# Optimization experiments

Measured on AMD Instinct MI355X. Metric: run time of the kernel, lower is better.

Reference implementation:

```python
import jax, jax.numpy as jnp
import numpy as np

T, B, D, H = 1024, 512, 128, 256


def setup_inputs() -> dict:
    key = jax.random.key(0)
    k0, k1, k2, k3, k4, k5 = jax.random.split(key, 6)
    data = jax.random.normal(k0, (T, B, D), dtype=jnp.float32)
    # ragged lengths in [1, T]; masked recurrence == packed-sequence semantics
    lengths = jax.random.randint(k1, (B,), 1, T + 1, dtype=jnp.int32)
    s_ih = 1.0 / np.sqrt(D)
    s_hh = 1.0 / np.sqrt(H)
    ih_w = jax.random.uniform(k2, (H, D), minval=-s_ih, maxval=s_ih, dtype=jnp.float32)
    ih_b = jax.random.uniform(k3, (H,), minval=-s_ih, maxval=s_ih, dtype=jnp.float32)
    hh_w = jax.random.uniform(k4, (2 * H, H), minval=-s_hh, maxval=s_hh, dtype=jnp.float32)
    hh_b = jax.random.uniform(k5, (2 * H,), minval=-s_hh, maxval=s_hh, dtype=jnp.float32)
    return {"data": data, "ih_w": ih_w, "ih_b": ih_b, "hh_w": hh_w, "hh_b": hh_b, "lengths": lengths}


def reference(data, ih_w, ih_b, hh_w, hh_b, lengths):
    # data: [T, B, D]; masked update replicates packed-sequence 'first size rows' semantics
    Tn, Bn, _ = data.shape
    Hn = ih_w.shape[0]

    def step(hidden, inp):
        x_t, t = inp
        hid = hidden @ hh_w.T + hh_b                    # [B, 2H]
        alpha, h = jnp.split(hid, 2, axis=1)
        alpha = jax.nn.sigmoid(alpha)
        h = (jnp.exp2(alpha * h) - 1.0) / alpha + alpha  # soft-exp gate
        new_hidden = jnp.tanh(x_t @ ih_w.T + ih_b + h)   # [B, H]
        valid = (t < lengths)[:, None]
        return jnp.where(valid, new_hidden, hidden), None

    h0 = jnp.zeros((Bn, Hn), dtype=data.dtype)
    hidden, _ = jax.lax.scan(step, h0, (data, jnp.arange(Tn)))
    return hidden[None]  # [1, B, H], matching hidden.unsqueeze(0)
```

## Files before the change

### kernel.cpp

```cpp
#include <hip/hip_runtime.h>


#define BB 512
#define DD 128
#define HH 256

typedef __attribute__((ext_vector_type(8))) short bf16x8;
typedef __attribute__((ext_vector_type(4))) float f32x4;

static __device__ __forceinline__ short f2bf(float f) {
    unsigned u = __float_as_uint(f);
    u += 0x7FFFu + ((u >> 16) & 1u);
    return (short)(u >> 16);
}
static __device__ __forceinline__ bf16x8 pack8(const float4 a, const float4 b) {
    bf16x8 v;
    v[0] = f2bf(a.x); v[1] = f2bf(a.y); v[2] = f2bf(a.z); v[3] = f2bf(a.w);
    v[4] = f2bf(b.x); v[5] = f2bf(b.y); v[6] = f2bf(b.z); v[7] = f2bf(b.w);
    return v;
}

__global__ __launch_bounds__(1024, 4)
void rnn_fused(const float* __restrict__ data, const float* __restrict__ ih_w,
               const float* __restrict__ ih_b, const float* __restrict__ hh_w,
               const float* __restrict__ hh_b, const int* __restrict__ lengths,
               float* __restrict__ out)
{
    const int g    = blockIdx.x;
    const int tid  = threadIdx.x;
    const int w    = tid >> 6;
    const int lane = tid & 63;
    const int col  = lane & 15;
    const int quad = lane >> 4;

    __shared__ short hbuf[2][32][4][8];
    __shared__ short dbuf[2][2][DD];

    bf16x8 whh[2][8];
    #pragma unroll
    for (int s = 0; s < 2; ++s) {
        const int wrow = s*HH + 16*w + col;
        const float* src = hh_w + wrow * HH;
        #pragma unroll
        for (int i = 0; i < 8; ++i) {
            const float4 a = *(const float4*)(src + i*32 + quad*8);
            const float4 b = *(const float4*)(src + i*32 + quad*8 + 4);
            whh[s][i] = pack8(a, b);
        }
    }
    bf16x8 wih[4];
    {
        const int wrow = 16*w + col;
        const float* src = ih_w + wrow * DD;
        #pragma unroll
        for (int i = 0; i < 4; ++i) {
            const float4 a = *(const float4*)(src + i*32 + quad*8);
            const float4 b = *(const float4*)(src + i*32 + quad*8 + 4);
            wih[i] = pack8(a, b);
        }
    }

    const float bA = hh_b[      16*w + col];
    const float bH = hh_b[HH  + 16*w + col];
    const float bX = ih_b[      16*w + col];

    const int L0 = lengths[2*g];
    const int L1 = lengths[2*g + 1];
    const int Lmax = (L0 > L1) ? L0 : L1;

    const bool smine = (quad == 0);
    const int  se    = (w << 4) | col;

    for (int idx = tid; idx < 32*4*8; idx += 1024)
        ((short*)hbuf[0])[idx] = 0;
    if (smine)
        ((short*)dbuf[0])[se] = f2bf(data[(size_t)(2*g) * DD + se]);
    float vstage = 0.f;
    if (smine && 1 < Lmax)
        vstage = data[((size_t)1 * BB + 2*g) * DD + se];
    __syncthreads();

    float  nh[2] = {0.f, 0.f};
    bf16x8 frag[4] = {};

    const bool acth = (col < 4);
    const bool actd = (col < 2);

    for (int t = 0; t < Lmax; ++t) {
        const int p = t & 1;

        if (smine && t + 1 < Lmax)
            ((short*)dbuf[1 - p])[se] = f2bf(vstage);
        float vnew = 0.f;
        if (smine && t + 2 < Lmax)
            vnew = data[((size_t)(t+2) * BB + 2*g) * DD + se];

        f32x4 racc[2] = {{0.f,0.f,0.f,0.f},{0.f,0.f,0.f,0.f}};
        #pragma unroll
        for (int half = 0; half < 2; ++half) {
            if (acth) {
                #pragma unroll
                for (int i = 0; i < 4; ++i)
                    frag[i] = *(const bf16x8*)
                        &hbuf[p][(half*4 + i)*4 + quad][col][0];
            }
            #pragma unroll
            for (int i = 0; i < 4; ++i)
                #pragma unroll
                for (int s = 0; s < 2; ++s)
                    racc[s] = __builtin_amdgcn_mfma_f32_16x16x32_bf16(
                        frag[i], whh[s][half*4 + i], racc[s], 0, 0, 0);
        }

        if (actd) {
            #pragma unroll
            for (int i = 0; i < 4; ++i)
                frag[i] = *(const bf16x8*)&dbuf[p][col][i*32 + quad*8];
        }
        f32x4 xacc = {0.f, 0.f, 0.f, 0.f};
        #pragma unroll
        for (int i = 0; i < 4; ++i)
            xacc = __builtin_amdgcn_mfma_f32_16x16x32_bf16(
                frag[i], wih[i], xacc, 0, 0, 0);

        float vres[2];
        #pragma unroll
        for (int r = 0; r < 2; ++r) {
            const float a   = racc[0][r] + racc[0][2 + r] + bA;
            const float hv  = racc[1][r] + racc[1][2 + r] + bH;
            const float e   = __builtin_amdgcn_exp2f(a * -1.4426950408889634f);
            const float inv = 1.0f + e;
            const float al  = __builtin_amdgcn_rcpf(inv);
            const float xs  = xacc[r] + bX;
            const float c1  = al + xs - inv;
            const float pp  = __builtin_amdgcn_exp2f(al * hv);
            const float u   = __builtin_fmaf(pp, inv, c1);
            const float t2  = __builtin_amdgcn_exp2f(u * 2.8853900817779268f);
            const float th  = 1.0f - 2.0f * __builtin_amdgcn_rcpf(1.0f + t2);
            const int   Lr  = r ? L1 : L0;
            vres[r] = (t < Lr) ? th : nh[r];
            nh[r]   = vres[r];
        }

        unsigned pkhi, pklo;
        asm("v_cvt_pk_bf16_f32 %0, %1, %2"
            : "=v"(pkhi) : "v"(vres[0]), "v"(vres[1]));
        const float b0 = __uint_as_float(pkhi << 16);
        const float b1 = __uint_as_float(pkhi & 0xFFFF0000u);
        asm("v_cvt_pk_bf16_f32 %0, %1, %2"
            : "=v"(pklo) : "v"(vres[0] - b0), "v"(vres[1] - b1));
        if (quad == 0) {
            const int c = 16*w + col;
            short* hb = &hbuf[1 - p][c >> 3][0][c & 7];
            hb[0]  = (short)(pkhi & 0xFFFFu);
            hb[8]  = (short)(pkhi >> 16);
            hb[16] = (short)(pklo & 0xFFFFu);
            hb[24] = (short)(pklo >> 16);
        }

        vstage = vnew;
        __syncthreads();
    }

    if (quad == 0) {
        #pragma unroll
        for (int r = 0; r < 2; ++r)
            out[(size_t)(2*g + r) * HH + 16*w + col] = nh[r];
    }
}

extern "C" void kernel_launch(void* const* d_in, const int* in_sizes, int n_in,
                              void* d_out, int out_size, void* d_ws, size_t ws_size,
                              hipStream_t stream) {
    const float* data    = (const float*)d_in[0];
    const float* ih_w    = (const float*)d_in[1];
    const float* ih_b    = (const float*)d_in[2];
    const float* hh_w    = (const float*)d_in[3];
    const float* hh_b    = (const float*)d_in[4];
    const int*   lengths = (const int*)d_in[5];
    float* out = (float*)d_out;

    (void)in_sizes; (void)n_in; (void)out_size; (void)d_ws; (void)ws_size;

    rnn_fused<<<dim3(BB / 2), dim3(1024), 0, stream>>>(
        data, ih_w, ih_b, hh_w, hh_b, lengths, out);
}
```

Before: 1.341 ms.

## Split per-row gate math across quads via swizzle, add MFMA priority and lighter barrier

The element-wise activation chain, which ran serially for two batch rows in quad 0 of each wave, is now split so quads 0 and 1 each handle one row. A ds_swizzle moves the second row's accumulator values across lanes, which halves the transcendental latency on the recurrent critical path. MFMA sections are wrapped in s_setprio, and __syncthreads is replaced by an explicit lgkmcnt wait plus s_barrier to cut barrier overhead. The cost is extra swizzle instructions, and the hand-written barrier relies on correct waitcnt semantics.

```diff
diff --git a/kernel.cpp b/kernel.cpp
--- a/kernel.cpp
+++ b/kernel.cpp
@@ -18,6 +18,10 @@
     v[0] = f2bf(a.x); v[1] = f2bf(a.y); v[2] = f2bf(a.z); v[3] = f2bf(a.w);
     v[4] = f2bf(b.x); v[5] = f2bf(b.y); v[6] = f2bf(b.z); v[7] = f2bf(b.w);
     return v;
+}
+static __device__ __forceinline__ float swz16(float x) {
+    return __uint_as_float((unsigned)__builtin_amdgcn_ds_swizzle(
+        (int)__float_as_uint(x), 0x401F));
 }
 
 __global__ __launch_bounds__(1024, 4)
@@ -80,11 +84,13 @@
         vstage = data[((size_t)1 * BB + 2*g) * DD + se];
     __syncthreads();
 
-    float  nh[2] = {0.f, 0.f};
+    float  nhv = 0.f;
     bf16x8 frag[4] = {};
 
     const bool acth = (col < 4);
     const bool actd = (col < 2);
+    const int  rq   = quad & 1;
+    const int  Lr   = rq ? L1 : L0;
 
     for (int t = 0; t < Lmax; ++t) {
         const int p = t & 1;
@@ -96,6 +102,7 @@
             vnew = data[((size_t)(t+2) * BB + 2*g) * DD + se];
 
         f32x4 racc[2] = {{0.f,0.f,0.f,0.f},{0.f,0.f,0.f,0.f}};
+        __builtin_amdgcn_s_setprio(1);
         #pragma unroll
         for (int half = 0; half < 2; ++half) {
             if (acth) {
@@ -122,51 +129,49 @@
         for (int i = 0; i < 4; ++i)
             xacc = __builtin_amdgcn_mfma_f32_16x16x32_bf16(
                 frag[i], wih[i], xacc, 0, 0, 0);
+        __builtin_amdgcn_s_setprio(0);
 
-        float vres[2];
-        #pragma unroll
-        for (int r = 0; r < 2; ++r) {
-            const float a   = racc[0][r] + racc[0][2 + r] + bA;
-            const float hv  = racc[1][r] + racc[1][2 + r] + bH;
-            const float e   = __builtin_amdgcn_exp2f(a * -1.4426950408889634f);
-            const float inv = 1.0f + e;
-            const float al  = __builtin_amdgcn_rcpf(inv);
-            const float xs  = xacc[r] + bX;
-            const float c1  = al + xs - inv;
-            const float pp  = __builtin_amdgcn_exp2f(al * hv);
-            const float u   = __builtin_fmaf(pp, inv, c1);
-            const float t2  = __builtin_amdgcn_exp2f(u * 2.8853900817779268f);
-            const float th  = 1.0f - 2.0f * __builtin_amdgcn_rcpf(1.0f + t2);
-            const int   Lr  = r ? L1 : L0;
-            vres[r] = (t < Lr) ? th : nh[r];
-            nh[r]   = vres[r];
-        }
+        const float a0 = racc[0][0] + racc[0][2];
+        const float a1 = racc[0][1] + racc[0][3];
+        const float h0 = racc[1][0] + racc[1][2];
+        const float h1 = racc[1][1] + racc[1][3];
+        const float x0 = xacc[0];
+        const float x1 = xacc[1];
+        const float a1s = swz16(a1);
+        const float h1s = swz16(h1);
+        const float x1s = swz16(x1);
+        const float a  = (rq ? a1s : a0) + bA;
+        const float hv = (rq ? h1s : h0) + bH;
+        const float xs = (rq ? x1s : x0) + bX;
 
-        unsigned pkhi, pklo;
-        asm("v_cvt_pk_bf16_f32 %0, %1, %2"
-            : "=v"(pkhi) : "v"(vres[0]), "v"(vres[1]));
-        const float b0 = __uint_as_float(pkhi << 16);
-        const float b1 = __uint_as_float(pkhi & 0xFFFF0000u);
-        asm("v_cvt_pk_bf16_f32 %0, %1, %2"
-            : "=v"(pklo) : "v"(vres[0] - b0), "v"(vres[1] - b1));
-        if (quad == 0) {
+        const float e   = __builtin_amdgcn_exp2f(a * -1.4426950408889634f);
+        const float inv = 1.0f + e;
+        const float al  = __builtin_amdgcn_rcpf(inv);
+        const float c1  = al + xs - inv;
+        const float pp  = __builtin_amdgcn_exp2f(al * hv);
+        const float u   = __builtin_fmaf(pp, inv, c1);
+        const float t2  = __builtin_amdgcn_exp2f(u * 2.8853900817779268f);
+        const float th  = 1.0f - 2.0f * __builtin_amdgcn_rcpf(1.0f + t2);
+        const float v   = (t < Lr) ? th : nhv;
+        nhv = v;
+
+        unsigned pk, pk2;
+        asm("v_cvt_pk_bf16_f32 %0, %1, %1" : "=v"(pk)  : "v"(v));
+        const float bhi = __uint_as_float(pk << 16);
+        asm("v_cvt_pk_bf16_f32 %0, %1, %1" : "=v"(pk2) : "v"(v - bhi));
+        if (quad < 2) {
             const int c = 16*w + col;
-            short* hb = &hbuf[1 - p][c >> 3][0][c & 7];
-            hb[0]  = (short)(pkhi & 0xFFFFu);
-            hb[8]  = (short)(pkhi >> 16);
-            hb[16] = (short)(pklo & 0xFFFFu);
-            hb[24] = (short)(pklo >> 16);
+            hbuf[1 - p][c >> 3][rq    ][c & 7] = (short)pk;
+            hbuf[1 - p][c >> 3][2 + rq][c & 7] = (short)pk2;
         }
 
         vstage = vnew;
-        __syncthreads();
+        asm volatile("s_waitcnt lgkmcnt(0)" ::: "memory");
+        __builtin_amdgcn_s_barrier();
     }
 
-    if (quad == 0) {
-        #pragma unroll
-        for (int r = 0; r < 2; ++r)
-            out[(size_t)(2*g + r) * HH + 16*w + col] = nh[r];
-    }
+    if (quad < 2)
+        out[(size_t)(2*g + rq) * HH + 16*w + col] = nhv;
 }
 
 extern "C" void kernel_launch(void* const* d_in, const int* in_sizes, int n_in,
```

Result: faster. 1.274 ms (-5.0%).
